# Optimization experiments

Hardware: AMD Instinct MI355X
Metric: run time of the kernel (lower is better)

## Reference

```python
import jax, jax.numpy as jnp
import numpy as np

N_EXPERTS = 16
IN_DIM = 1024
OUT_DIM = 1024
BATCH = 4096

def setup_inputs() -> dict:
    key = jax.random.key(0)
    k1, k2, k3, k4 = jax.random.split(key, 4)
    x = jax.random.normal(k1, (BATCH, IN_DIM), dtype=jnp.float32)
    comp_weight = jax.random.uniform(k2, (BATCH, N_EXPERTS), dtype=jnp.float32)
    # torch.rand init (uniform [0,1)) per original module
    weight = jax.random.uniform(k3, (N_EXPERTS, IN_DIM, OUT_DIM), dtype=jnp.float32)
    bias = jax.random.uniform(k4, (N_EXPERTS, OUT_DIM), dtype=jnp.float32)
    return {"x": x, "comp_weight": comp_weight, "weight": weight, "bias": bias}

def reference(x, comp_weight, weight, bias):
    # z[n,b,o] = x[b,i] @ weight[n,i,o] + bias[n,o]   (baddbmm)
    z = jnp.einsum('bi,nio->nbo', x, weight) + bias[:, None, :]
    # out[b,o] = sum_n comp_weight[b,n] * z[n,b,o]    (bmm combine)
    out = jnp.einsum('bn,nbo->bo', comp_weight, z)
    return jax.nn.relu(out)
```

## Files before the change

### kernel.cpp

```cpp
#include <hip/hip_runtime.h>
#include <hip/hip_bf16.h>
#include <cstdint>

#define BATCH   4096
#define IN_DIM  1024
#define OUT_DIM 1024
#define NEXP    16

typedef __bf16 bf16;
typedef __attribute__((ext_vector_type(8))) __bf16 bf16x8;
typedef __attribute__((ext_vector_type(4))) float  f32x4;

#define AS1 __attribute__((address_space(1)))
#define AS3 __attribute__((address_space(3)))

__device__ __forceinline__ void gld_lds16(const bf16* g, bf16* l) {
    __builtin_amdgcn_global_load_lds((const AS1 void*)g, (AS3 void*)l, 16, 0, 0);
}

__global__ __launch_bounds__(256) void convert_all(
        const float* __restrict__ x, const float* __restrict__ W,
        bf16* __restrict__ xt, bf16* __restrict__ wt) {
    __shared__ float Ls[64][65];
    int t = threadIdx.x;
    int bid = blockIdx.x;
    if (bid < 4096) {
        int nblk = bid >> 8, ne = (bid >> 4) & 15, ks = bid & 15;
        int kb = ne * 1024 + ks * 64;
        int n0 = nblk * 64;
#pragma unroll
        for (int r = 0; r < 4; r++) {
            int idx = r * 256 + t;
            int row = idx >> 4, c4 = (idx & 15) * 4;
            f32x4 v = *(const f32x4*)(W + (size_t)(kb + row) * OUT_DIM + n0 + c4);
#pragma unroll
            for (int j = 0; j < 4; j++) Ls[row][c4 + j] = v[j];
        }
        __syncthreads();
#pragma unroll
        for (int r = 0; r < 2; r++) {
            int c = r * 256 + t;
            int sub = c >> 6, l = c & 63;
            int lr = l & 15, lq = l >> 4;
            int kk = sub >> 2, wn = (sub >> 1) & 1, nt = sub & 1;
            int krow = kk * 32 + lq * 8;
            int col = wn * 32 + nt * 16 + lr;
            bf16x8 v;
#pragma unroll
            for (int j = 0; j < 8; j++) v[j] = (bf16)Ls[krow + j][col];
            *(bf16x8*)(wt + (size_t)bid * 4096 + c * 8) = v;
        }
    } else {
        int tile = bid - 4096;
        int mblk = tile >> 4, ks = tile & 15;
#pragma unroll
        for (int r = 0; r < 4; r++) {
            int q = r * 256 + t;
            int m_loc = q >> 3, sc = q & 7;
            int cc = sc ^ (m_loc & 7);
            const float* src = x + (size_t)(mblk * 128 + m_loc) * IN_DIM + ks * 64 + cc * 8;
            f32x4 a = *(const f32x4*)src;
            f32x4 b = *(const f32x4*)(src + 4);
            bf16x8 v;
#pragma unroll
            for (int j = 0; j < 4; j++) { v[j] = (bf16)a[j]; v[4 + j] = (bf16)b[j]; }
            *(bf16x8*)(xt + (size_t)tile * 8192 + q * 8) = v;
        }
    }
}

__global__ __launch_bounds__(256, 2) void moe_gemm(
        const float* __restrict__ cw, const float* __restrict__ bias,
        const bf16* __restrict__ xt, const bf16* __restrict__ wt,
        float* __restrict__ out) {
    int nblk = blockIdx.x;
    int mblk = blockIdx.y;
    int m0 = mblk * 128, n0 = nblk * 64;
    int t = threadIdx.x;
    int lane = t & 63, w = t >> 6;
    int wm = w >> 1, wn = w & 1;
    int lq = lane >> 4, lr = lane & 15;

    __shared__ bf16 As[128 * 64];
    __shared__ bf16 Bs[4][64 * 64];
    __shared__ float cwS[128][20];

#pragma unroll
    for (int r = 0; r < 2; r++) {
        int q = r * 256 + t;
        f32x4 v = *(const f32x4*)(cw + (size_t)m0 * NEXP + q * 4);
        *(f32x4*)&cwS[q >> 2][(q & 3) * 4] = v;
    }

    const f32x4 fz = {0.f, 0.f, 0.f, 0.f};
    f32x4 acc[4][2];
#pragma unroll
    for (int mt = 0; mt < 4; mt++)
#pragma unroll
        for (int nt = 0; nt < 2; nt++) acc[mt][nt] = fz;

    int swz = lr & 7;
    int mrow[4];
#pragma unroll
    for (int mt = 0; mt < 4; mt++) mrow[mt] = (wm * 64 + mt * 16 + lr) * 64;

    const bf16* abase = xt + (size_t)(mblk * 16) * 8192;
    const bf16* bbase = wt + (size_t)nblk * (16 * 16 * 4096);

#pragma unroll 1
    for (int ks = 0; ks < 16; ks++) {
        const bf16* asrc = abase + (size_t)ks * 8192 + t * 8;
#pragma unroll
        for (int r = 0; r < 4; r++) gld_lds16(asrc + r * 2048, &As[r * 2048 + t * 8]);
        const bf16* b0 = bbase + (size_t)ks * 4096 + t * 8;
        gld_lds16(b0,        &Bs[0][t * 8]);
        gld_lds16(b0 + 2048, &Bs[0][2048 + t * 8]);
        const bf16* b1 = bbase + (size_t)(16 + ks) * 4096 + t * 8;
        gld_lds16(b1,        &Bs[1][t * 8]);
        gld_lds16(b1 + 2048, &Bs[1][2048 + t * 8]);
        __syncthreads();

        bf16x8 af[4][2];
#pragma unroll
        for (int kk = 0; kk < 2; kk++)
#pragma unroll
            for (int mt = 0; mt < 4; mt++)
                af[mt][kk] = *(const bf16x8*)&As[mrow[mt] + ((kk * 4 + lq) ^ swz) * 8];

        f32x4 sg[4];
#pragma unroll
        for (int ne = 0; ne < 16; ne++) {
            if ((ne & 3) == 0) {
#pragma unroll
                for (int mt = 0; mt < 4; mt++)
                    sg[mt] = *(const f32x4*)&cwS[wm * 64 + mt * 16 + lr][ne];
            }
            if ((ne & 1) == 0 && ne < 14) {
                const bf16* bn2 = bbase + (size_t)((ne + 2) * 16 + ks) * 4096 + t * 8;
                bf16* bd2 = &Bs[(ne + 2) & 3][t * 8];
                gld_lds16(bn2,        bd2);
                gld_lds16(bn2 + 2048, bd2 + 2048);
                const bf16* bn3 = bbase + (size_t)((ne + 3) * 16 + ks) * 4096 + t * 8;
                bf16* bd3 = &Bs[(ne + 3) & 3][t * 8];
                gld_lds16(bn3,        bd3);
                gld_lds16(bn3 + 2048, bd3 + 2048);
            }
            bf16x8 bfr[2][2];
#pragma unroll
            for (int kk = 0; kk < 2; kk++)
#pragma unroll
                for (int nt = 0; nt < 2; nt++)
                    bfr[kk][nt] = *(const bf16x8*)
                        &Bs[ne & 3][((kk * 2 + wn) * 2 + nt) * 512 + lane * 8];
#pragma unroll
            for (int mt = 0; mt < 4; mt++) {
                float sv = sg[mt][ne & 3];
#pragma unroll
                for (int nt = 0; nt < 2; nt++) {
                    f32x4 p = __builtin_amdgcn_mfma_f32_16x16x32_bf16(
                        bfr[0][nt], af[mt][0], fz, 0, 0, 0);
                    p = __builtin_amdgcn_mfma_f32_16x16x32_bf16(
                        bfr[1][nt], af[mt][1], p, 0, 0, 0);
                    acc[mt][nt] += sv * p;
                }
            }
            if (ne & 1) __syncthreads();
        }
    }

    {
        bf16x8 acw[4];
#pragma unroll
        for (int mt = 0; mt < 4; mt++) {
            bf16x8 v;
#pragma unroll
            for (int j = 0; j < 8; j++) v[j] = (bf16)0.f;
            if (lq < 2) {
                int row = m0 + wm * 64 + mt * 16 + lr;
                f32x4 a = *(const f32x4*)(cw + (size_t)row * NEXP + lq * 8);
                f32x4 b = *(const f32x4*)(cw + (size_t)row * NEXP + lq * 8 + 4);
#pragma unroll
                for (int j = 0; j < 4; j++) { v[j] = (bf16)a[j]; v[4 + j] = (bf16)b[j]; }
            }
            acw[mt] = v;
        }
        bf16x8 bb[2];
#pragma unroll
        for (int nt = 0; nt < 2; nt++) {
            bf16x8 v;
#pragma unroll
            for (int j = 0; j < 8; j++) v[j] = (bf16)0.f;
            if (lq < 2) {
                int col = n0 + wn * 32 + nt * 16 + lr;
#pragma unroll
                for (int j = 0; j < 8; j++)
                    v[j] = (bf16)bias[(size_t)(lq * 8 + j) * OUT_DIM + col];
            }
            bb[nt] = v;
        }
#pragma unroll
        for (int mt = 0; mt < 4; mt++)
#pragma unroll
            for (int nt = 0; nt < 2; nt++)
                acc[mt][nt] = __builtin_amdgcn_mfma_f32_16x16x32_bf16(
                    bb[nt], acw[mt], acc[mt][nt], 0, 0, 0);
    }

#pragma unroll
    for (int mt = 0; mt < 4; mt++) {
        int row = m0 + wm * 64 + mt * 16 + lr;
#pragma unroll
        for (int nt = 0; nt < 2; nt++) {
            int col = n0 + wn * 32 + nt * 16 + lq * 4;
            f32x4 v = acc[mt][nt];
#pragma unroll
            for (int r2 = 0; r2 < 4; r2++) v[r2] = v[r2] > 0.f ? v[r2] : 0.f;
            *(f32x4*)(out + (size_t)row * OUT_DIM + col) = v;
        }
    }
}

__global__ void fallback_kernel(const float* __restrict__ x, const float* __restrict__ cw,
                                const float* __restrict__ W, const float* __restrict__ bias,
                                float* __restrict__ out) {
    int o = blockIdx.x * 256 + threadIdx.x;
    int b = o >> 10, oc = o & 1023;
    const float* xr = x + (size_t)b * IN_DIM;
    float accv = 0.f;
    for (int n = 0; n < NEXP; n++) {
        const float* wr = W + (size_t)n * IN_DIM * OUT_DIM + oc;
        float z = 0.f;
        for (int i = 0; i < IN_DIM; i++) z += xr[i] * wr[(size_t)i * OUT_DIM];
        accv += cw[(size_t)b * NEXP + n] * (z + bias[n * OUT_DIM + oc]);
    }
    out[o] = accv > 0.f ? accv : 0.f;
}

extern "C" void kernel_launch(void* const* d_in, const int* in_sizes, int n_in,
                              void* d_out, int out_size, void* d_ws, size_t ws_size,
                              hipStream_t stream) {
    const float* x    = (const float*)d_in[0];
    const float* cw   = (const float*)d_in[1];
    const float* W    = (const float*)d_in[2];
    const float* bias = (const float*)d_in[3];
    float* out = (float*)d_out;

    const size_t wt_elems = (size_t)NEXP * IN_DIM * OUT_DIM;
    const size_t xt_elems = (size_t)BATCH * IN_DIM;
    if (ws_size < (wt_elems + xt_elems) * sizeof(bf16)) {
        fallback_kernel<<<(BATCH * OUT_DIM) / 256, 256, 0, stream>>>(x, cw, W, bias, out);
        return;
    }
    bf16* wt = (bf16*)d_ws;
    bf16* xt = wt + wt_elems;

    convert_all<<<4096 + 512, 256, 0, stream>>>(x, W, xt, wt);
    moe_gemm<<<dim3(16, 32), 256, 0, stream>>>(cw, bias, xt, wt, out);
}
```

Baseline: 241.7 us.

## Load A and B fragments directly from global memory instead of staging through LDS

```diff
diff --git a/kernel.cpp b/kernel.cpp
--- a/kernel.cpp
+++ b/kernel.cpp
@@ -13,10 +13,6 @@
 
 #define AS1 __attribute__((address_space(1)))
 #define AS3 __attribute__((address_space(3)))
-
-__device__ __forceinline__ void gld_lds16(const bf16* g, bf16* l) {
-    __builtin_amdgcn_global_load_lds((const AS1 void*)g, (AS3 void*)l, 16, 0, 0);
-}
 
 __global__ __launch_bounds__(256) void convert_all(
         const float* __restrict__ x, const float* __restrict__ W,
@@ -81,8 +77,6 @@
     int wm = w >> 1, wn = w & 1;
     int lq = lane >> 4, lr = lane & 15;
 
-    __shared__ bf16 As[128 * 64];
-    __shared__ bf16 Bs[4][64 * 64];
     __shared__ float cwS[128][20];
 
 #pragma unroll
@@ -91,6 +85,7 @@
         f32x4 v = *(const f32x4*)(cw + (size_t)m0 * NEXP + q * 4);
         *(f32x4*)&cwS[q >> 2][(q & 3) * 4] = v;
     }
+    __syncthreads();
 
     const f32x4 fz = {0.f, 0.f, 0.f, 0.f};
     f32x4 acc[4][2];
@@ -105,66 +100,49 @@
     for (int mt = 0; mt < 4; mt++) mrow[mt] = (wm * 64 + mt * 16 + lr) * 64;
 
     const bf16* abase = xt + (size_t)(mblk * 16) * 8192;
-    const bf16* bbase = wt + (size_t)nblk * (16 * 16 * 4096);
+    const bf16* bbase = wt + (size_t)nblk * (16 * 16 * 4096) + lane * 8;
+    const float* cwrow0 = &cwS[wm * 64 + lr][0];
 
 #pragma unroll 1
     for (int ks = 0; ks < 16; ks++) {
-        const bf16* asrc = abase + (size_t)ks * 8192 + t * 8;
-#pragma unroll
-        for (int r = 0; r < 4; r++) gld_lds16(asrc + r * 2048, &As[r * 2048 + t * 8]);
-        const bf16* b0 = bbase + (size_t)ks * 4096 + t * 8;
-        gld_lds16(b0,        &Bs[0][t * 8]);
-        gld_lds16(b0 + 2048, &Bs[0][2048 + t * 8]);
-        const bf16* b1 = bbase + (size_t)(16 + ks) * 4096 + t * 8;
-        gld_lds16(b1,        &Bs[1][t * 8]);
-        gld_lds16(b1 + 2048, &Bs[1][2048 + t * 8]);
-        __syncthreads();
-
         bf16x8 af[4][2];
+        const bf16* asrc = abase + (size_t)ks * 8192;
 #pragma unroll
         for (int kk = 0; kk < 2; kk++)
 #pragma unroll
             for (int mt = 0; mt < 4; mt++)
-                af[mt][kk] = *(const bf16x8*)&As[mrow[mt] + ((kk * 4 + lq) ^ swz) * 8];
-
-        f32x4 sg[4];
-#pragma unroll
-        for (int ne = 0; ne < 16; ne++) {
-            if ((ne & 3) == 0) {
-#pragma unroll
-                for (int mt = 0; mt < 4; mt++)
-                    sg[mt] = *(const f32x4*)&cwS[wm * 64 + mt * 16 + lr][ne];
-            }
-            if ((ne & 1) == 0 && ne < 14) {
-                const bf16* bn2 = bbase + (size_t)((ne + 2) * 16 + ks) * 4096 + t * 8;
-                bf16* bd2 = &Bs[(ne + 2) & 3][t * 8];
-                gld_lds16(bn2,        bd2);
-                gld_lds16(bn2 + 2048, bd2 + 2048);
-                const bf16* bn3 = bbase + (size_t)((ne + 3) * 16 + ks) * 4096 + t * 8;
-                bf16* bd3 = &Bs[(ne + 3) & 3][t * 8];
-                gld_lds16(bn3,        bd3);
-                gld_lds16(bn3 + 2048, bd3 + 2048);
-            }
-            bf16x8 bfr[2][2];
-#pragma unroll
-            for (int kk = 0; kk < 2; kk++)
-#pragma unroll
-                for (int nt = 0; nt < 2; nt++)
-                    bfr[kk][nt] = *(const bf16x8*)
-                        &Bs[ne & 3][((kk * 2 + wn) * 2 + nt) * 512 + lane * 8];
-#pragma unroll
-            for (int mt = 0; mt < 4; mt++) {
-                float sv = sg[mt][ne & 3];
-#pragma unroll
-                for (int nt = 0; nt < 2; nt++) {
-                    f32x4 p = __builtin_amdgcn_mfma_f32_16x16x32_bf16(
-                        bfr[0][nt], af[mt][0], fz, 0, 0, 0);
-                    p = __builtin_amdgcn_mfma_f32_16x16x32_bf16(
-                        bfr[1][nt], af[mt][1], p, 0, 0, 0);
-                    acc[mt][nt] += sv * p;
+                af[mt][kk] = *(const bf16x8*)
+                    (asrc + mrow[mt] + ((kk * 4 + lq) ^ swz) * 8);
+
+#pragma unroll 1
+        for (int ne4 = 0; ne4 < 4; ne4++) {
+            f32x4 sg[4];
+#pragma unroll
+            for (int mt = 0; mt < 4; mt++)
+                sg[mt] = *(const f32x4*)(cwrow0 + mt * (16 * 20) + ne4 * 4);
+#pragma unroll
+            for (int e = 0; e < 4; e++) {
+                const bf16* btile = bbase + (size_t)((ne4 * 4 + e) * 16 + ks) * 4096;
+                bf16x8 bfr[2][2];
+#pragma unroll
+                for (int kk = 0; kk < 2; kk++)
+#pragma unroll
+                    for (int nt = 0; nt < 2; nt++)
+                        bfr[kk][nt] = *(const bf16x8*)
+                            (btile + ((kk * 2 + wn) * 2 + nt) * 512);
+#pragma unroll
+                for (int mt = 0; mt < 4; mt++) {
+                    float sv = sg[mt][e];
+#pragma unroll
+                    for (int nt = 0; nt < 2; nt++) {
+                        f32x4 p = __builtin_amdgcn_mfma_f32_16x16x32_bf16(
+                            bfr[0][nt], af[mt][0], fz, 0, 0, 0);
+                        p = __builtin_amdgcn_mfma_f32_16x16x32_bf16(
+                            bfr[1][nt], af[mt][1], p, 0, 0, 0);
+                        acc[mt][nt] += sv * p;
+                    }
                 }
             }
-            if (ne & 1) __syncthreads();
         }
     }
 
```

After: 255.2 us. +5.6%, slower.
